# Performance work log

Measured on AMD Instinct MI355X. Metric: run time of the kernel, lower is better.

The kernel has to match this reference:

```python
import jax, jax.numpy as jnp
import numpy as np

HIDDEN = 512
HEADS = 8
HEAD_DIM = HIDDEN // HEADS
THRESH = 0.1
EPS = 1e-8


def setup_inputs() -> dict:
    key = jax.random.key(0)
    ks = jax.random.split(key, 9)
    B, S = 2, 4096
    scale = 1.0 / np.sqrt(HIDDEN)
    x = jax.random.normal(ks[0], (B, S, HIDDEN), dtype=jnp.float32)
    Wq = jax.random.normal(ks[1], (HIDDEN, HIDDEN), dtype=jnp.float32) * scale
    bq = jnp.zeros((HIDDEN,), dtype=jnp.float32)
    Wk = jax.random.normal(ks[2], (HIDDEN, HIDDEN), dtype=jnp.float32) * scale
    bk = jnp.zeros((HIDDEN,), dtype=jnp.float32)
    Wv = jax.random.normal(ks[3], (HIDDEN, HIDDEN), dtype=jnp.float32) * scale
    bv = jnp.zeros((HIDDEN,), dtype=jnp.float32)
    Wo = jax.random.normal(ks[4], (HIDDEN, HIDDEN), dtype=jnp.float32) * scale
    bo = jnp.zeros((HIDDEN,), dtype=jnp.float32)
    return {"x": x, "Wq": Wq, "bq": bq, "Wk": Wk, "bk": bk,
            "Wv": Wv, "bv": bv, "Wo": Wo, "bo": bo}


def reference(x, Wq, bq, Wk, bk, Wv, bv, Wo, bo):
    B, S, _ = x.shape
    # torch Linear: y = x @ W.T + b
    def proj(W, b):
        y = jnp.einsum('bsd,ed->bse', x, W) + b
        return y.reshape(B, S, HEADS, HEAD_DIM).transpose(0, 2, 1, 3)  # [B,H,S,Dh]
    Q = proj(Wq, bq)
    K = proj(Wk, bk)
    V = proj(Wv, bv)
    scores = jnp.einsum('bhqd,bhkd->bhqk', Q, K) / jnp.sqrt(jnp.float32(HEAD_DIM))
    probs = jax.nn.softmax(scores, axis=-1)  # [B,H,S,S]
    probs = jnp.where(probs > THRESH, probs, 0.0)
    probs = probs / (jnp.sum(probs, axis=-1, keepdims=True) + EPS)
    ctx = jnp.einsum('bhqk,bhkd->bhqd', probs, V)
    ctx = ctx.transpose(0, 2, 1, 3).reshape(B, S, HIDDEN)
    return jnp.einsum('bsd,ed->bse', ctx, Wo) + bo
```

## Files before the change

kernel.cpp:

```cpp
#include <hip/hip_runtime.h>

#define S_LEN 4096
#define BATCH 2
#define HID 512
#define HEADS 8
#define HD 64
#define NX (BATCH * S_LEN * HID)
#define WSZ (HID * HID)
#define NBH (BATCH * HEADS)
#define QB 64
#define NBLK (S_LEN / QB * NBH)

typedef short v8s __attribute__((ext_vector_type(8)));
typedef float v4f __attribute__((ext_vector_type(4)));
typedef float v16f __attribute__((ext_vector_type(16)));
typedef unsigned short ushort_t;

__device__ __forceinline__ ushort_t f2bf(float f) {
  unsigned u = __builtin_bit_cast(unsigned, f);
  u += 0x7fffu + ((u >> 16) & 1u);
  return (ushort_t)(u >> 16);
}
__device__ __forceinline__ unsigned pk2(float a, float b) {
  return (__builtin_bit_cast(unsigned, a) >> 16) |
         (__builtin_bit_cast(unsigned, b) & 0xFFFF0000u);
}
__device__ __forceinline__ float fexp2(float x) {
  return __builtin_amdgcn_exp2f(x);
}


__global__ __launch_bounds__(256) void cvt_k(
    const float* __restrict__ x,
    const float* __restrict__ wq, const float* __restrict__ wk,
    const float* __restrict__ wv, const float* __restrict__ wo,
    ushort_t* __restrict__ dst)
{
  const size_t e = ((size_t)blockIdx.x * 256 + threadIdx.x) * 4;
  const float* src; size_t off;
  if (e < NX) { src = x; off = e; }
  else {
    const size_t we = e - NX;
    const int wi = (int)(we >> 18);
    src = wi == 0 ? wq : wi == 1 ? wk : wi == 2 ? wv : wo;
    off = we & (WSZ - 1);
  }
  float4 v = *(const float4*)&src[off];
  uint2 u; u.x = pk2(v.x, v.y); u.y = pk2(v.z, v.w);
  *(uint2*)&dst[e] = u;
}

__global__ __launch_bounds__(256) void gemm_qkv(
    const ushort_t* __restrict__ X, const ushort_t* __restrict__ Wb,
    const float* __restrict__ bq, const float* __restrict__ bk, const float* __restrict__ bv,
    ushort_t* __restrict__ Qf, ushort_t* __restrict__ Kf, ushort_t* __restrict__ Vw,
    float qscale)
{
  __shared__ ushort_t As[128][40];
  __shared__ ushort_t Bs[128][40];
  const int t = threadIdx.x;
  const int lane = t & 63;
  const int l15 = lane & 15, lg = lane >> 4;
  const int w = t >> 6;
  const int wr = w >> 1, wc = w & 1;
  const int m0 = blockIdx.y * 128;
  const int wsel = blockIdx.x >> 2;
  const int e0 = (blockIdx.x & 3) * 128;
  const ushort_t* W = Wb + (size_t)wsel * WSZ;
  const float* bias = wsel == 0 ? bq : wsel == 1 ? bk : bv;
  const float osc = (wsel == 0) ? qscale : 1.0f;

  v4f acc[4][4] = {};
  const int srow = t >> 2, scol = (t & 3) * 8;

  for (int k0 = 0; k0 < HID; k0 += 32) {
    __syncthreads();
    #pragma unroll
    for (int rep = 0; rep < 2; ++rep) {
      *(uint4*)&As[srow + rep * 64][scol] =
          *(const uint4*)&X[(size_t)(m0 + srow + rep * 64) * HID + k0 + scol];
      *(uint4*)&Bs[srow + rep * 64][scol] =
          *(const uint4*)&W[(size_t)(e0 + srow + rep * 64) * HID + k0 + scol];
    }
    __syncthreads();
    v8s a[4], b[4];
    #pragma unroll
    for (int fr = 0; fr < 4; ++fr)
      a[fr] = *(const v8s*)&As[wr * 64 + 16 * fr + l15][8 * lg];
    #pragma unroll
    for (int fc = 0; fc < 4; ++fc)
      b[fc] = *(const v8s*)&Bs[wc * 64 + 16 * fc + l15][8 * lg];
    #pragma unroll
    for (int fr = 0; fr < 4; ++fr)
      #pragma unroll
      for (int fc = 0; fc < 4; ++fc)
        acc[fr][fc] = __builtin_amdgcn_mfma_f32_16x16x32_bf16(a[fr], b[fc], acc[fr][fc], 0, 0, 0);
  }

  #pragma unroll
  for (int fr = 0; fr < 4; ++fr)
    #pragma unroll
    for (int fc = 0; fc < 4; ++fc) {
      const int e = e0 + wc * 64 + 16 * fc + l15;
      const float bval = bias[e];
      #pragma unroll
      for (int r = 0; r < 4; ++r) {
        const int m = m0 + wr * 64 + 16 * fr + 4 * lg + r;
        const float v = (acc[fr][fc][r] + bval) * osc;
        const int bidx = m >> 12, s = m & (S_LEN - 1);
        const int hh = e >> 6, dh = e & 63;
        const size_t hb = ((size_t)(bidx * HEADS + hh)) * (size_t)(S_LEN * HD);
        if (wsel == 2) {
          Vw[hb + (size_t)s * HD + dh] = f2bf(v);
        } else {
          const size_t off = (size_t)(s >> 5) * 2048 +
              (size_t)(((dh >> 4) * 64 + ((dh >> 3) & 1) * 32 + (s & 31)) * 8 + (dh & 7));
          (wsel == 0 ? Qf : Kf)[hb + off] = f2bf(v);
        }
      }
    }
}

__global__ __launch_bounds__(256, 3) void attn_p1(
    const ushort_t* __restrict__ Qf, const ushort_t* __restrict__ Kf,
    ushort_t* __restrict__ Cb, int* __restrict__ Flg)
{
  __shared__ float RedL[4][QB];
  __shared__ float RedM[4][QB];
  __shared__ int bflag;
  const int t = threadIdx.x;
  const int lane = t & 63;
  const int l31 = lane & 31, hi = lane >> 5;
  const int w = t >> 6;
  const int lin = blockIdx.x;
  const int bh = ((lin & 7) << 1) | ((lin >> 3) & 1);
  const int q0 = (lin >> 4) * QB;
  if (t == 0) bflag = 0;

  const size_t hoff = (size_t)bh * (size_t)(S_LEN * HD);
  const ushort_t* Qb = Qf + hoff + (size_t)(q0 >> 5) * 2048;
  const ushort_t* Kb = Kf + hoff;

  v8s qa[4], qB[4];
  #pragma unroll
  for (int ks = 0; ks < 4; ++ks) {
    qa[ks] = *(const v8s*)&Qb[(ks * 64 + lane) * 8];
    qB[ks] = *(const v8s*)&Qb[2048 + (ks * 64 + lane) * 8];
  }

  float L0[16], L1[16], M0[16], M1[16];
  #pragma unroll
  for (int j = 0; j < 16; ++j) {
    L0[j] = 0.f; L1[j] = 0.f; M0[j] = -1e30f; M1[j] = -1e30f;
  }

  for (int i = 0; i < 32; ++i) {
    const ushort_t* kc = Kb + (size_t)(w + 4 * i) * 2048;
    v8s kb[4];
    #pragma unroll
    for (int ks = 0; ks < 4; ++ks)
      kb[ks] = *(const v8s*)&kc[(ks * 64 + lane) * 8];
    v16f sa = {}, sb = {};
    #pragma unroll
    for (int ks = 0; ks < 4; ++ks)
      sa = __builtin_amdgcn_mfma_f32_32x32x16_bf16(qa[ks], kb[ks], sa, 0, 0, 0);
    #pragma unroll
    for (int ks = 0; ks < 4; ++ks)
      sb = __builtin_amdgcn_mfma_f32_32x32x16_bf16(qB[ks], kb[ks], sb, 0, 0, 0);
    #pragma unroll
    for (int j = 0; j < 16; ++j) {
      M0[j] = fmaxf(M0[j], sa[j]);
      L0[j] += fexp2(sa[j]);
    }
    #pragma unroll
    for (int j = 0; j < 16; ++j) {
      M1[j] = fmaxf(M1[j], sb[j]);
      L1[j] += fexp2(sb[j]);
    }
  }

  #pragma unroll
  for (int rs = 0; rs < 2; ++rs)
    #pragma unroll
    for (int j = 0; j < 16; ++j) {
      float Lv = (rs == 0) ? L0[j] : L1[j];
      float Mv = (rs == 0) ? M0[j] : M1[j];
      Lv += __shfl_xor(Lv, 1);  Mv = fmaxf(Mv, __shfl_xor(Mv, 1));
      Lv += __shfl_xor(Lv, 2);  Mv = fmaxf(Mv, __shfl_xor(Mv, 2));
      Lv += __shfl_xor(Lv, 4);  Mv = fmaxf(Mv, __shfl_xor(Mv, 4));
      Lv += __shfl_xor(Lv, 8);  Mv = fmaxf(Mv, __shfl_xor(Mv, 8));
      Lv += __shfl_xor(Lv, 16); Mv = fmaxf(Mv, __shfl_xor(Mv, 16));
      if (l31 == 0) {
        const int row = rs * 32 + (j & 3) + 8 * (j >> 2) + 4 * hi;
        RedL[w][row] = Lv;
        RedM[w][row] = Mv;
      }
    }
  __syncthreads();
  if (t < QB) {
    const float Lv = RedL[0][t] + RedL[1][t] + RedL[2][t] + RedL[3][t];
    const float Mv = fmaxf(fmaxf(RedM[0][t], RedM[1][t]),
                           fmaxf(RedM[2][t], RedM[3][t]));
    if (Mv >= __log2f(Lv) - 3.3719281f) atomicOr(&bflag, 1);
  }
  __syncthreads();
  if (t == 0) Flg[lin] = bflag;

  const int b = bh >> 3, h = bh & 7;
  const uint4 z = {0u, 0u, 0u, 0u};
  #pragma unroll
  for (int rep = 0; rep < 2; ++rep) {
    const int row = (t >> 3) + rep * 32;
    const int d8 = (t & 7) * 8;
    *(uint4*)&Cb[((size_t)b * S_LEN + q0 + row) * HID + h * HD + d8] = z;
  }
}

__global__ __launch_bounds__(256) void attn_p2(
    const ushort_t* __restrict__ Qf, const ushort_t* __restrict__ Kf,
    const ushort_t* __restrict__ V, ushort_t* __restrict__ Cb,
    const int* __restrict__ Flg)
{
  const int lin = blockIdx.x;
  if (Flg[lin] == 0) return;
  __shared__ float Osh[QB][HD + 1];
  __shared__ float Dsh[QB];
  __shared__ float RedA[4][QB];
  __shared__ float iLs[QB];
  __shared__ ushort_t Pp[4][32][40];
  __shared__ ushort_t VT[4][HD][40];
  const int t = threadIdx.x;
  const int lane = t & 63;
  const int l31 = lane & 31, hi = lane >> 5;
  const int w = t >> 6;
  const int bh = ((lin & 7) << 1) | ((lin >> 3) & 1);
  const int q0 = (lin >> 4) * QB;
  const size_t hoff = (size_t)bh * (size_t)(S_LEN * HD);
  const ushort_t* Qb = Qf + hoff + (size_t)(q0 >> 5) * 2048;
  const ushort_t* Kb = Kf + hoff;
  const ushort_t* Vh = V + hoff;

  if (t < QB) Dsh[t] = 0.f;
  for (int idx = t; idx < QB * HD; idx += 256) Osh[idx >> 6][idx & 63] = 0.f;

  v8s qa[4], qB[4];
  #pragma unroll
  for (int ks = 0; ks < 4; ++ks) {
    qa[ks] = *(const v8s*)&Qb[(ks * 64 + lane) * 8];
    qB[ks] = *(const v8s*)&Qb[2048 + (ks * 64 + lane) * 8];
  }

  float L0[16], L1[16];
  #pragma unroll
  for (int j = 0; j < 16; ++j) { L0[j] = 0.f; L1[j] = 0.f; }
  for (int i = 0; i < 32; ++i) {
    const ushort_t* kc = Kb + (size_t)(w + 4 * i) * 2048;
    v8s kb[4];
    #pragma unroll
    for (int ks = 0; ks < 4; ++ks)
      kb[ks] = *(const v8s*)&kc[(ks * 64 + lane) * 8];
    v16f sa = {}, sb = {};
    #pragma unroll
    for (int ks = 0; ks < 4; ++ks) {
      sa = __builtin_amdgcn_mfma_f32_32x32x16_bf16(qa[ks], kb[ks], sa, 0, 0, 0);
      sb = __builtin_amdgcn_mfma_f32_32x32x16_bf16(qB[ks], kb[ks], sb, 0, 0, 0);
    }
    #pragma unroll
    for (int j = 0; j < 16; ++j) {
      L0[j] += fexp2(sa[j]);
      L1[j] += fexp2(sb[j]);
    }
  }
  #pragma unroll
  for (int rseti = 0; rseti < 2; ++rseti)
    #pragma unroll
    for (int j = 0; j < 16; ++j) {
      float Lv = (rseti == 0) ? L0[j] : L1[j];
      Lv += __shfl_xor(Lv, 1);  Lv += __shfl_xor(Lv, 2);
      Lv += __shfl_xor(Lv, 4);  Lv += __shfl_xor(Lv, 8);
      Lv += __shfl_xor(Lv, 16);
      if (l31 == 0) {
        const int row = rseti * 32 + (j & 3) + 8 * (j >> 2) + 4 * hi;
        RedA[w][row] = Lv;
      }
    }
  __syncthreads();
  if (t < QB)
    iLs[t] = 1.0f / (RedA[0][t] + RedA[1][t] + RedA[2][t] + RedA[3][t]);
  __syncthreads();

  float il[2][16];
  #pragma unroll
  for (int rseti = 0; rseti < 2; ++rseti)
    #pragma unroll
    for (int j = 0; j < 16; ++j)
      il[rseti][j] = iLs[rseti * 32 + (j & 3) + 8 * (j >> 2) + 4 * hi];

  v16f oA[2] = {}, oB[2] = {};
  float den[2][16] = {};

  for (int i = 0; i < 32; ++i) {
    const int c = w + 4 * i;
    const ushort_t* kc = Kb + (size_t)c * 2048;
    v8s kb[4];
    #pragma unroll
    for (int ks = 0; ks < 4; ++ks)
      kb[ks] = *(const v8s*)&kc[(ks * 64 + lane) * 8];
    v16f sa = {}, sb = {};
    #pragma unroll
    for (int ks = 0; ks < 4; ++ks) {
      sa = __builtin_amdgcn_mfma_f32_32x32x16_bf16(qa[ks], kb[ks], sa, 0, 0, 0);
      sb = __builtin_amdgcn_mfma_f32_32x32x16_bf16(qB[ks], kb[ks], sb, 0, 0, 0);
    }
    {
      const ushort_t* vsrc = &Vh[((size_t)c * 32 + l31) * HD + hi * 32];
      #pragma unroll
      for (int qq = 0; qq < 4; ++qq) {
        uint4 vv = *(const uint4*)&vsrc[qq * 8];
        const ushort_t* pv = (const ushort_t*)&vv;
        #pragma unroll
        for (int jj = 0; jj < 8; ++jj)
          VT[w][hi * 32 + qq * 8 + jj][l31] = pv[jj];
      }
    }
    #pragma unroll
    for (int rseti = 0; rseti < 2; ++rseti) {
      #pragma unroll
      for (int j = 0; j < 16; ++j) {
        const float s = (rseti == 0) ? sa[j] : sb[j];
        const int row = (j & 3) + 8 * (j >> 2) + 4 * hi;
        float p = fexp2(s) * il[rseti][j];
        p = (p > 0.1f) ? p : 0.f;
        den[rseti][j] += p;
        Pp[w][row][l31] = f2bf(p);
      }
      v8s pa0 = *(const v8s*)&Pp[w][l31][8 * hi];
      v8s pa1 = *(const v8s*)&Pp[w][l31][16 + 8 * hi];
      #pragma unroll
      for (int dblk = 0; dblk < 2; ++dblk) {
        v8s vb0 = *(const v8s*)&VT[w][dblk * 32 + l31][8 * hi];
        v8s vb1 = *(const v8s*)&VT[w][dblk * 32 + l31][16 + 8 * hi];
        if (rseti == 0) {
          oA[dblk] = __builtin_amdgcn_mfma_f32_32x32x16_bf16(pa0, vb0, oA[dblk], 0, 0, 0);
          oA[dblk] = __builtin_amdgcn_mfma_f32_32x32x16_bf16(pa1, vb1, oA[dblk], 0, 0, 0);
        } else {
          oB[dblk] = __builtin_amdgcn_mfma_f32_32x32x16_bf16(pa0, vb0, oB[dblk], 0, 0, 0);
          oB[dblk] = __builtin_amdgcn_mfma_f32_32x32x16_bf16(pa1, vb1, oB[dblk], 0, 0, 0);
        }
      }
    }
  }

  #pragma unroll
  for (int rseti = 0; rseti < 2; ++rseti)
    #pragma unroll
    for (int j = 0; j < 16; ++j) {
      float d = den[rseti][j];
      d += __shfl_xor(d, 1); d += __shfl_xor(d, 2); d += __shfl_xor(d, 4);
      d += __shfl_xor(d, 8); d += __shfl_xor(d, 16);
      const int row = rseti * 32 + (j & 3) + 8 * (j >> 2) + 4 * hi;
      if (l31 == 0) atomicAdd(&Dsh[row], d);
    }
  #pragma unroll
  for (int rseti = 0; rseti < 2; ++rseti)
    #pragma unroll
    for (int dblk = 0; dblk < 2; ++dblk)
      #pragma unroll
      for (int j = 0; j < 16; ++j) {
        const int row = rseti * 32 + (j & 3) + 8 * (j >> 2) + 4 * hi;
        const float val = (rseti == 0) ? oA[dblk][j] : oB[dblk][j];
        atomicAdd(&Osh[row][dblk * 32 + l31], val);
      }
  __syncthreads();
  const int b = bh >> 3, h = bh & 7;
  for (int idx = t; idx < QB * HD; idx += 256) {
    const int row = idx >> 6, d = idx & 63;
    const float val = Osh[row][d] / (Dsh[row] + 1e-8f);
    Cb[((size_t)b * S_LEN + q0 + row) * HID + h * HD + d] = f2bf(val);
  }
}

__global__ __launch_bounds__(256) void gemm_out(
    const ushort_t* __restrict__ X, const ushort_t* __restrict__ W,
    const float* __restrict__ bias, const int* __restrict__ Flg,
    float* __restrict__ Df)
{
  const int t = threadIdx.x;
  const int m0 = blockIdx.y * 64;
  const int e0 = blockIdx.x * 64;

  {
    const int b = m0 >> 12, qblk = (m0 & (S_LEN - 1)) >> 6;
    int any = 0;
    #pragma unroll
    for (int h = 0; h < HEADS; ++h) {
      const int bhh = b * HEADS + h;
      any |= Flg[(bhh >> 1) | ((bhh & 1) << 3) | (qblk << 4)];
    }
    if (!any) {
      const int row = t >> 2, c0 = (t & 3) * 16;
      #pragma unroll
      for (int g = 0; g < 4; ++g) {
        const float4 bv = *(const float4*)&bias[e0 + c0 + g * 4];
        *(float4*)&Df[(size_t)(m0 + row) * HID + e0 + c0 + g * 4] = bv;
      }
      return;
    }
  }

  __shared__ ushort_t As[64][40];
  __shared__ ushort_t Bs[64][40];
  const int lane = t & 63;
  const int l15 = lane & 15, lg = lane >> 4;
  const int w = t >> 6;
  const int wr = w >> 1, wc = w & 1;

  v4f acc[2][2] = {};
  const int srow = t >> 2, scol = (t & 3) * 8;

  for (int k0 = 0; k0 < HID; k0 += 32) {
    __syncthreads();
    *(uint4*)&As[srow][scol] =
        *(const uint4*)&X[(size_t)(m0 + srow) * HID + k0 + scol];
    *(uint4*)&Bs[srow][scol] =
        *(const uint4*)&W[(size_t)(e0 + srow) * HID + k0 + scol];
    __syncthreads();
    v8s a[2], b[2];
    #pragma unroll
    for (int fr = 0; fr < 2; ++fr)
      a[fr] = *(const v8s*)&As[wr * 32 + 16 * fr + l15][8 * lg];
    #pragma unroll
    for (int fc = 0; fc < 2; ++fc)
      b[fc] = *(const v8s*)&Bs[wc * 32 + 16 * fc + l15][8 * lg];
    #pragma unroll
    for (int fr = 0; fr < 2; ++fr)
      #pragma unroll
      for (int fc = 0; fc < 2; ++fc)
        acc[fr][fc] = __builtin_amdgcn_mfma_f32_16x16x32_bf16(a[fr], b[fc], acc[fr][fc], 0, 0, 0);
  }

  #pragma unroll
  for (int fr = 0; fr < 2; ++fr)
    #pragma unroll
    for (int fc = 0; fc < 2; ++fc) {
      const int e = e0 + wc * 32 + 16 * fc + l15;
      const float bval = bias[e];
      #pragma unroll
      for (int r = 0; r < 4; ++r) {
        const int m = m0 + wr * 32 + 16 * fr + 4 * lg + r;
        Df[(size_t)m * HID + e] = acc[fr][fc][r] + bval;
      }
    }
}

extern "C" void kernel_launch(void* const* d_in, const int* in_sizes, int n_in,
                              void* d_out, int out_size, void* d_ws, size_t ws_size,
                              hipStream_t stream) {
  const float* x  = (const float*)d_in[0];
  const float* Wq = (const float*)d_in[1];
  const float* bq = (const float*)d_in[2];
  const float* Wk = (const float*)d_in[3];
  const float* bk = (const float*)d_in[4];
  const float* Wv = (const float*)d_in[5];
  const float* bv = (const float*)d_in[6];
  const float* Wo = (const float*)d_in[7];
  const float* bo = (const float*)d_in[8];

  int*      Flg  = (int*)d_ws;
  ushort_t* xb   = (ushort_t*)(Flg + NBLK);
  ushort_t* wqb  = xb + NX;
  ushort_t* wob  = wqb + 3 * WSZ;
  ushort_t* Qf   = wob + WSZ;
  ushort_t* Kf   = Qf + NX;
  ushort_t* Vw   = Kf + NX;
  ushort_t* Cb   = Vw + NX;

  const float qscale = 0.125f * 1.44269504f;

  cvt_k<<<(NX + 4 * WSZ) / 1024, 256, 0, stream>>>(x, Wq, Wk, Wv, Wo, xb);

  gemm_qkv<<<dim3(12, 64), 256, 0, stream>>>(
      xb, wqb, bq, bk, bv, Qf, Kf, Vw, qscale);

  attn_p1<<<NBLK, 256, 0, stream>>>(Qf, Kf, Cb, Flg);
  attn_p2<<<NBLK, 256, 0, stream>>>(Qf, Kf, Vw, Cb, Flg);

  gemm_out<<<dim3(8, 128), 256, 0, stream>>>(Cb, wob, bo, Flg, (float*)d_out);
}
```

Measured before the change: 115.7 us.

## Split attention pass-1 over key halves and reduce row stats in separate kernel

```diff
diff --git a/kernel.cpp b/kernel.cpp
--- a/kernel.cpp
+++ b/kernel.cpp
@@ -121,25 +121,25 @@
     }
 }
 
-__global__ __launch_bounds__(256, 3) void attn_p1(
+__global__ __launch_bounds__(256, 4) void attn_p1(
     const ushort_t* __restrict__ Qf, const ushort_t* __restrict__ Kf,
-    ushort_t* __restrict__ Cb, int* __restrict__ Flg)
+    ushort_t* __restrict__ Cb, float2* __restrict__ Part)
 {
   __shared__ float RedL[4][QB];
   __shared__ float RedM[4][QB];
-  __shared__ int bflag;
   const int t = threadIdx.x;
   const int lane = t & 63;
   const int l31 = lane & 31, hi = lane >> 5;
   const int w = t >> 6;
-  const int lin = blockIdx.x;
+  const int nlin = blockIdx.x;
+  const int khalf = nlin & 1;
+  const int lin = nlin >> 1;
   const int bh = ((lin & 7) << 1) | ((lin >> 3) & 1);
   const int q0 = (lin >> 4) * QB;
-  if (t == 0) bflag = 0;
 
   const size_t hoff = (size_t)bh * (size_t)(S_LEN * HD);
   const ushort_t* Qb = Qf + hoff + (size_t)(q0 >> 5) * 2048;
-  const ushort_t* Kb = Kf + hoff;
+  const ushort_t* Kb = Kf + hoff + (size_t)khalf * 64 * 2048;
 
   v8s qa[4], qB[4];
   #pragma unroll
@@ -154,7 +154,7 @@
     L0[j] = 0.f; L1[j] = 0.f; M0[j] = -1e30f; M1[j] = -1e30f;
   }
 
-  for (int i = 0; i < 32; ++i) {
+  for (int i = 0; i < 16; ++i) {
     const ushort_t* kc = Kb + (size_t)(w + 4 * i) * 2048;
     v8s kb[4];
     #pragma unroll
@@ -201,19 +201,36 @@
     const float Lv = RedL[0][t] + RedL[1][t] + RedL[2][t] + RedL[3][t];
     const float Mv = fmaxf(fmaxf(RedM[0][t], RedM[1][t]),
                            fmaxf(RedM[2][t], RedM[3][t]));
-    if (Mv >= __log2f(Lv) - 3.3719281f) atomicOr(&bflag, 1);
-  }
-  __syncthreads();
-  if (t == 0) Flg[lin] = bflag;
-
-  const int b = bh >> 3, h = bh & 7;
-  const uint4 z = {0u, 0u, 0u, 0u};
-  #pragma unroll
-  for (int rep = 0; rep < 2; ++rep) {
-    const int row = (t >> 3) + rep * 32;
-    const int d8 = (t & 7) * 8;
-    *(uint4*)&Cb[((size_t)b * S_LEN + q0 + row) * HID + h * HD + d8] = z;
-  }
+    float2 p; p.x = Lv; p.y = Mv;
+    Part[((size_t)lin * 2 + khalf) * QB + t] = p;
+  }
+
+  if (khalf == 0) {
+    const int b = bh >> 3, h = bh & 7;
+    const uint4 z = {0u, 0u, 0u, 0u};
+    #pragma unroll
+    for (int rep = 0; rep < 2; ++rep) {
+      const int row = (t >> 3) + rep * 32;
+      const int d8 = (t & 7) * 8;
+      *(uint4*)&Cb[((size_t)b * S_LEN + q0 + row) * HID + h * HD + d8] = z;
+    }
+  }
+}
+
+__global__ __launch_bounds__(256) void attn_red(
+    const float2* __restrict__ Part, int* __restrict__ Flg)
+{
+  const int t = threadIdx.x;
+  const int r = blockIdx.x * 256 + t;
+  const int logical = r >> 6;
+  const int row = r & 63;
+  const float2 a = Part[((size_t)logical * 2 + 0) * QB + row];
+  const float2 b = Part[((size_t)logical * 2 + 1) * QB + row];
+  const float L = a.x + b.x;
+  const float M = fmaxf(a.y, b.y);
+  const bool pred = (M >= __log2f(L) - 3.3719281f);
+  const unsigned long long m = __ballot(pred);
+  if ((t & 63) == 0) Flg[logical] = (m != 0ull) ? 1 : 0;
 }
 
 __global__ __launch_bounds__(256) void attn_p2(
@@ -467,7 +484,8 @@
   const float* bo = (const float*)d_in[8];
 
   int*      Flg  = (int*)d_ws;
-  ushort_t* xb   = (ushort_t*)(Flg + NBLK);
+  float2*   Part = (float2*)(Flg + NBLK);
+  ushort_t* xb   = (ushort_t*)(Part + 2 * NBLK * QB);
   ushort_t* wqb  = xb + NX;
   ushort_t* wob  = wqb + 3 * WSZ;
   ushort_t* Qf   = wob + WSZ;
@@ -482,7 +500,8 @@
   gemm_qkv<<<dim3(12, 64), 256, 0, stream>>>(
       xb, wqb, bq, bk, bv, Qf, Kf, Vw, qscale);
 
-  attn_p1<<<NBLK, 256, 0, stream>>>(Qf, Kf, Cb, Flg);
+  attn_p1<<<2 * NBLK, 256, 0, stream>>>(Qf, Kf, Cb, Part);
+  attn_red<<<NBLK * QB / 256, 256, 0, stream>>>(Part, Flg);
   attn_p2<<<NBLK, 256, 0, stream>>>(Qf, Kf, Vw, Cb, Flg);
 
   gemm_out<<<dim3(8, 128), 256, 0, stream>>>(Cb, wob, bo, Flg, (float*)d_out);
```

New measurement: 126.9 us. +9.6%, slower.
